# Optimization experiments

Hardware: AMD Instinct MI355X
Metric: run time of the kernel (lower is better)

Reference implementation:

```python
import jax, jax.numpy as jnp
from jax import lax
import numpy as np

EPS = 0.1          # DBSCAN radius (init arg eps)
MIN_SAMPLES = 5    # DBSCAN min_samples (init arg min_samples)
NC_MAX = 512       # fixed padded cluster budget (8 per dim * 64 dims)


def _dbscan_1d(x):
    """Exact 1-D DBSCAN on a vector x of shape (N,).
    Returns (labels, n_clusters). labels[i] in [-1, n_clusters), -1 = noise.
    Clusters are numbered in ascending value order (canonical deterministic
    relabeling of sklearn's discovery order). Border points are attached to
    the nearest core point (ties -> left)."""
    n = x.shape[0]
    order = jnp.argsort(x)
    xs = x[order]
    # core test: #points within [xs-eps, xs+eps] >= min_samples
    hi = jnp.searchsorted(xs, xs + EPS, side='right')
    lo = jnp.searchsorted(xs, xs - EPS, side='left')
    core = (hi - lo) >= MIN_SAMPLES
    inf = jnp.inf
    core_vals = jnp.where(core, xs, -inf)
    run_max = lax.cummax(core_vals, axis=0)                 # nearest core value to the left (incl self)
    prev_core_val = jnp.concatenate([jnp.full((1,), -inf, xs.dtype), run_max[:-1]])
    # a core point starts a new cluster iff no core point within eps on its left
    new_cluster = core & ((xs - prev_core_val) > EPS)
    starts = jnp.cumsum(new_cluster.astype(jnp.int32))
    cid = starts - 1                                        # cluster id carried along sorted order
    ncl = starts[-1]
    # nearest core on the left / right (values and their cluster ids)
    left_cid = lax.cummax(jnp.where(core, cid, -1), axis=0)
    left_val = run_max
    right_cid = lax.cummin(jnp.where(core, cid, n + 1), axis=0, reverse=True)
    right_val = lax.cummin(jnp.where(core, xs, inf), axis=0, reverse=True)
    dl = xs - left_val
    dr = right_val - xs
    border_cid = jnp.where(dl <= dr, left_cid, right_cid)
    border_ok = jnp.minimum(dl, dr) <= EPS
    lab_sorted = jnp.where(core, cid, jnp.where(border_ok, border_cid, -1))
    labels = jnp.zeros_like(lab_sorted).at[order].set(lab_sorted)  # unsort to original node order
    return labels, ncl


def setup_inputs() -> dict:
    key = jax.random.key(0)
    features = jax.random.normal(key, (8, 16384, 64), dtype=jnp.float32)
    return {"features": features}


def reference(features):
    B, N, D = features.shape
    xt = jnp.transpose(features, (0, 2, 1))                  # (B, D, N)
    labels, ncl = jax.vmap(jax.vmap(_dbscan_1d))(xt)         # (B, D, N), (B, D)
    off = jnp.cumsum(ncl, axis=1) - ncl                      # exclusive prefix: global cluster offset per dim
    glb = jnp.where(labels >= 0, labels + off[:, :, None], -1)
    # noise / overflow -> dump into padding column NC_MAX, sliced off below
    lbl = jnp.where(glb >= 0, jnp.minimum(glb, NC_MAX), NC_MAX)
    inc = jnp.zeros((B, N, NC_MAX + 1), features.dtype)
    b_ix = jnp.arange(B)[:, None, None]
    n_ix = jnp.arange(N)[None, None, :]
    inc = inc.at[b_ix, n_ix, lbl].set(1.0)                   # scatter cluster membership
    return inc[:, :, :NC_MAX]                                # (B, N, NC_MAX) padded incidence matrix
```

## Files before the change

### kernel.cpp

```cpp
#include <hip/hip_runtime.h>

#define NPTS   16384
#define NDIM   64
#define NBATCH 8
#define TB     1024
#define VPT    16
#define NB     6144
#define BPT    6
#define NW     (NB/2)
#define EPSF   0.1f
#define MINS   5
#define NCMAX  512
#define BIGI   0x3fffffff

__device__ __forceinline__ int phys(int i) { return i ^ ((i >> 5) & 15); }

__device__ __forceinline__ int binof(float x, float mn, float inv) {
  float fb = (x - mn) * inv;
  int b = (int)fb;
  if (fb < 0.f) b = 0;
  if (b > NB - 1) b = NB - 1;
  return b;
}
__device__ __forceinline__ int pk_get(unsigned w, int odd) {
  return (int)((w >> (odd << 4)) & 0xffffu);
}

__global__ void ktrans(const float* __restrict__ f, float* __restrict__ xt) {
  __shared__ float tile[64][65];
  int blk = blockIdx.x;
  int b   = blk >> 8;
  int n0  = (blk & 255) << 6;
  for (int i = threadIdx.x; i < 64 * 64; i += 256) {
    int n = i >> 6, d = i & 63;
    tile[n][d] = f[((size_t)b * NPTS + n0 + n) * NDIM + d];
  }
  __syncthreads();
  for (int i = threadIdx.x; i < 64 * 64; i += 256) {
    int d = i >> 6, n = i & 63;
    xt[((size_t)b * NDIM + d) * NPTS + n0 + n] = tile[n][d];
  }
}

struct FS { int h; float f; float l; int c; };
__device__ __forceinline__ FS fsid() { FS r; r.h = 0; r.f = 0.f; r.l = 0.f; r.c = 0; return r; }
__device__ __forceinline__ FS fscomb(FS a, FS b) {
  FS r;
  r.h = a.h | b.h;
  r.f = a.h ? a.f : b.f;
  r.l = b.h ? b.l : a.l;
  int gap = (a.h && b.h && ((b.f - a.l) > EPSF)) ? 1 : 0;
  r.c = a.c + b.c + gap;
  return r;
}

__global__ void __launch_bounds__(TB) kdbscan(const float* __restrict__ xt,
                                              short* __restrict__ labels,
                                              int* __restrict__ nclg) {
  const int tid  = threadIdx.x;
  const int lane = tid & 63;
  const int wid  = tid >> 6;
  const int bd   = blockIdx.x;
  const float* __restrict__ x = xt + (size_t)bd * NPTS;

  __shared__ float xs[NPTS];
  __shared__ unsigned offsp[NW];
  __shared__ float wmn[16], wmx[16];
  __shared__ unsigned wsum[16];
  __shared__ int   sh[16];  __shared__ float sf[16], sl[16]; __shared__ int sc[16];
  __shared__ int   wri[16]; __shared__ float wrv[16];
  unsigned* histp = (unsigned*)xs;
  int* labi = (int*)xs;

  float v[VPT];
  float mn = INFINITY, mx = -INFINITY;
  #pragma unroll
  for (int s = 0; s < VPT; ++s) {
    v[s] = x[tid + s * TB];
    mn = fminf(mn, v[s]); mx = fmaxf(mx, v[s]);
  }
  for (int d = 1; d < 64; d <<= 1) {
    mn = fminf(mn, __shfl_xor(mn, d));
    mx = fmaxf(mx, __shfl_xor(mx, d));
  }
  if (lane == 0) { wmn[wid] = mn; wmx[wid] = mx; }
  __syncthreads();
  mn = wmn[0]; mx = wmx[0];
  for (int w = 1; w < 16; ++w) { mn = fminf(mn, wmn[w]); mx = fmaxf(mx, wmx[w]); }
  float range = mx - mn;
  float inv = (range > 0.f) ? ((float)NB / range) : 0.f;

  for (int i = tid; i < NW; i += TB) histp[i] = 0u;
  __syncthreads();
  #pragma unroll
  for (int s = 0; s < VPT; ++s) {
    int b = binof(v[s], mn, inv);
    atomicAdd(&histp[b >> 1], 1u << ((b & 1) << 4));
  }
  __syncthreads();

  {
    unsigned loc[BPT];
    unsigned run = 0;
    const int bbase = tid * BPT;
    #pragma unroll
    for (int j = 0; j < BPT; ++j) {
      int b = bbase + j;
      unsigned c = (histp[b >> 1] >> ((b & 1) << 4)) & 0xffffu;
      loc[j] = run; run += c;
    }
    unsigned incl = run;
    for (int d = 1; d < 64; d <<= 1) {
      unsigned u = __shfl_up(incl, d);
      if (lane >= d) incl += u;
    }
    unsigned exc = __shfl_up(incl, 1);
    if (lane == 0) exc = 0u;
    if (lane == 63) wsum[wid] = incl;
    __syncthreads();
    unsigned wb = 0;
    for (int w = 0; w < wid; ++w) wb += wsum[w];
    unsigned tb0 = wb + exc;
    #pragma unroll
    for (int k = 0; k < BPT / 2; ++k) {
      unsigned a  = tb0 + loc[2 * k];
      unsigned b2 = tb0 + loc[2 * k + 1];
      offsp[(bbase >> 1) + k] = a | (b2 << 16);
    }
  }
  __syncthreads();

  int pos[VPT];
  #pragma unroll
  for (int s = 0; s < VPT; ++s) {
    int b = binof(v[s], mn, inv);
    unsigned old = atomicAdd(&offsp[b >> 1], 1u << ((b & 1) << 4));
    int p = pk_get(old, b & 1);
    pos[s] = p;
    xs[phys(p)] = v[s];
  }
  __syncthreads();

  int tgt[VPT];
  #pragma unroll
  for (int s = 0; s < VPT; ++s) {
    float vv = v[s];
    int pp = pos[s];
    int b  = binof(vv, mn, inv);
    int e0 = pk_get(offsp[b >> 1], b & 1);
    int s0 = b ? pk_get(offsp[(b - 1) >> 1], (b - 1) & 1) : 0;
    int r = 0;
    for (int j = s0; j < e0; ++j) {
      float xj = xs[phys(j)];
      r += (xj < vv || (xj == vv && j < pp)) ? 1 : 0;
    }
    tgt[s] = s0 + r;
  }
  __syncthreads();

  #pragma unroll
  for (int s = 0; s < VPT; ++s) xs[phys(tgt[s])] = v[s];
  __syncthreads();

  const int p0 = tid * VPT;
  float wa[9];
  #pragma unroll
  for (int k = 0; k < 9; ++k) {
    int i = p0 - 4 + k;
    wa[k] = (i < 0) ? -INFINITY : xs[phys(i)];
  }
  unsigned coremask = 0u;
  FS ch = fsid();
  int fi = BIGI; float fv = 0.f;
  #pragma unroll
  for (int s = 0; s < VPT; ++s) {
    float xi = wa[4];
    float lo = xi - EPSF, hi2 = xi + EPSF;
    bool core = false;
    #pragma unroll
    for (int t = 0; t < MINS; ++t)
      core |= (wa[4 - t] >= lo) && (wa[8 - t] <= hi2);
    if (core) {
      coremask |= (1u << s);
      if (!ch.h) { ch.h = 1; ch.f = xi; }
      else if ((xi - ch.l) > EPSF) ++ch.c;
      ch.l = xi;
      if (fi == BIGI) { fi = p0 + s; fv = xi; }
    }
    #pragma unroll
    for (int k = 0; k < 8; ++k) wa[k] = wa[k + 1];
    int nx = p0 + s + 5;
    wa[8] = (nx < NPTS) ? xs[phys(nx)] : INFINITY;
  }

  FS cur = ch;
  for (int d = 1; d < 64; d <<= 1) {
    FS u;
    u.h = __shfl_up(cur.h, d);
    u.f = __shfl_up(cur.f, d);
    u.l = __shfl_up(cur.l, d);
    u.c = __shfl_up(cur.c, d);
    FS cmb = fscomb(u, cur);
    if (lane >= d) cur = cmb;
  }
  FS exs;
  exs.h = __shfl_up(cur.h, 1);
  exs.f = __shfl_up(cur.f, 1);
  exs.l = __shfl_up(cur.l, 1);
  exs.c = __shfl_up(cur.c, 1);
  if (lane == 0) exs = fsid();
  if (lane == 63) { sh[wid] = cur.h; sf[wid] = cur.f; sl[wid] = cur.l; sc[wid] = cur.c; }
  __syncthreads();
  FS pre = fsid();
  for (int w2 = 0; w2 < wid; ++w2) {
    FS t; t.h = sh[w2]; t.f = sf[w2]; t.l = sl[w2]; t.c = sc[w2];
    pre = fscomb(pre, t);
  }
  FS sp = fscomb(pre, exs);

  int ri = fi; float rv = fv;
  for (int d = 1; d < 64; d <<= 1) {
    int ui = __shfl_down(ri, d); float uv = __shfl_down(rv, d);
    if (lane < 64 - d && ui < ri) { ri = ui; rv = uv; }
  }
  int Ri = __shfl_down(ri, 1); float Rv = __shfl_down(rv, 1);
  if (lane == 63) Ri = BIGI;
  if (lane == 0) { wri[wid] = ri; wrv[wid] = rv; }
  __syncthreads();
  for (int w2 = wid + 1; w2 < 16; ++w2)
    if (wri[w2] < Ri) { Ri = wri[w2]; Rv = wrv[w2]; }

  float P  = sp.h ? sp.l : -INFINITY;
  int starts = sp.h ? (sp.c + 1) : 0;
  #pragma unroll
  for (int s = 0; s < VPT; ++s) {
    int i = p0 + s;
    float xi = xs[phys(i)];
    int lb;
    if ((coremask >> s) & 1u) {
      if ((xi - P) > EPSF) ++starts;
      P = xi;
      lb = starts - 1;
    } else {
      float dl = xi - P;
      unsigned hb = coremask >> (s + 1);
      float Rv2; bool has;
      if (hb) { int j = s + 1 + __builtin_ctz(hb); Rv2 = xs[phys(p0 + j)]; has = true; }
      else    { Rv2 = Rv; has = (Ri < NPTS); }
      float dr = has ? (Rv2 - xi) : INFINITY;
      lb = -1;
      if (fminf(dl, dr) <= EPSF)
        lb = (dl <= dr) ? (starts - 1)
                        : (starts - 1 + (((Rv2 - P) > EPSF) ? 1 : 0));
    }
    labi[phys(i)] = lb;
  }
  if (tid == TB - 1) nclg[bd] = starts;
  __syncthreads();

  #pragma unroll
  for (int s = 0; s < VPT; ++s)
    labels[(size_t)bd * NPTS + tid + s * TB] = (short)labi[phys(tgt[s])];
}

__global__ void koffs(const int* __restrict__ ncl, int* __restrict__ colmap) {
  int lane = threadIdx.x & 63;
  int b    = threadIdx.x >> 6;
  int vcnt = ncl[b * 64 + lane];
  int incl = vcnt;
  for (int d = 1; d < 64; d <<= 1) {
    int u = __shfl_up(incl, d);
    if (lane >= d) incl += u;
  }
  int off = incl - vcnt;
  int* cm = colmap + b * NCMAX;
  for (int k = lane; k < NCMAX; k += 64) cm[k] = -1;
  __syncthreads();
  for (int k = 0; k < vcnt; ++k) {
    int col = off + k;
    if (col < NCMAX) cm[col] = lane | (k << 8);
  }
}

__global__ void __launch_bounds__(TB) kout(const short* __restrict__ labels,
                                           const int* __restrict__ colmap,
                                           float* __restrict__ out) {
  const int tid  = threadIdx.x;
  const int lane = tid & 63;
  const int wid  = tid >> 6;
  const int b    = blockIdx.x >> 5;
  const int n0   = (blockIdx.x & 31) * 512 + wid * 32;

  int cm[8];
  const int* cmb = colmap + b * NCMAX;
  #pragma unroll
  for (int k = 0; k < 8; ++k) {
    int col = (k < 4) ? (lane * 4 + k) : (256 + lane * 4 + (k - 4));
    cm[k] = cmb[col];
  }
  const short* lb_b = labels + (size_t)b * NDIM * NPTS;

  for (int r = 0; r < 32; ++r) {
    int n = n0 + r;
    float o[8];
    #pragma unroll
    for (int k = 0; k < 8; ++k) {
      int m = cm[k];
      float val = 0.f;
      if (m >= 0) {
        int d  = m & 255;
        int kk = m >> 8;
        val = (lb_b[(size_t)d * NPTS + n] == (short)kk) ? 1.0f : 0.0f;
      }
      o[k] = val;
    }
    float4* op = (float4*)(out + ((size_t)b * NPTS + n) * NCMAX);
    op[lane]      = make_float4(o[0], o[1], o[2], o[3]);
    op[64 + lane] = make_float4(o[4], o[5], o[6], o[7]);
  }
}

extern "C" void kernel_launch(void* const* d_in, const int* in_sizes, int n_in,
                              void* d_out, int out_size, void* d_ws, size_t ws_size,
                              hipStream_t stream) {
  const float* feat = (const float*)d_in[0];
  float* out = (float*)d_out;

  char* ws = (char*)d_ws;
  size_t xt_b   = (size_t)NBATCH * NPTS * NDIM * 4;
  size_t lbl_b  = (size_t)NBATCH * NPTS * NDIM * 2;
  float* xt     = (float*)ws;
  short* labels = (short*)(ws + xt_b);
  int*   ncl    = (int*)(ws + xt_b + lbl_b);
  int*   colmap = ncl + NBATCH * NDIM;

  ktrans  <<<NBATCH * (NPTS / 64), 256, 0, stream>>>(feat, xt);
  kdbscan <<<NBATCH * NDIM, TB, 0, stream>>>(xt, labels, ncl);
  koffs   <<<1, 512, 0, stream>>>(ncl, colmap);
  kout    <<<NBATCH * 32, TB, 0, stream>>>(labels, colmap, out);
}
```

Before: 184.5 us.

## Fold cluster offset kernel into output kernel and enlarge histogram bins

Removes the separate single-block koffs launch. Each kout block now computes its batch's column map in LDS from the per-dimension cluster counts. The counting sort gets more bins (8192), so each bin holds fewer points and the in-bin rank scan is shorter. Shared memory is repacked so the small scratch arrays alias xs and the histogram array, with an extra barrier added. This adds redundant per-block prefix work in kout and relies on the aliasing being safe.

Result: faster. 179.0 us (-3.0%).

```diff
diff --git a/kernel.cpp b/kernel.cpp
--- a/kernel.cpp
+++ b/kernel.cpp
@@ -5,9 +5,10 @@
 #define NBATCH 8
 #define TB     1024
 #define VPT    16
-#define NB     6144
-#define BPT    6
+#define NB     8192
+#define BPT    8
 #define NW     (NB/2)
+#define WPT    4
 #define EPSF   0.1f
 #define MINS   5
 #define NCMAX  512
@@ -64,13 +65,17 @@
   const float* __restrict__ x = xt + (size_t)bd * NPTS;
 
   __shared__ float xs[NPTS];
-  __shared__ unsigned offsp[NW];
-  __shared__ float wmn[16], wmx[16];
-  __shared__ unsigned wsum[16];
-  __shared__ int   sh[16];  __shared__ float sf[16], sl[16]; __shared__ int sc[16];
-  __shared__ int   wri[16]; __shared__ float wrv[16];
-  unsigned* histp = (unsigned*)xs;
-  int* labi = (int*)xs;
+  __shared__ unsigned A[NW];
+  float*    wmn  = xs;
+  float*    wmx  = xs + 16;
+  unsigned* wsum = (unsigned*)xs + 32;
+  int*      sh   = (int*)A;
+  float*    sf   = (float*)A + 16;
+  float*    sl   = (float*)A + 32;
+  int*      sc   = (int*)A + 48;
+  int*      wri  = (int*)A + 64;
+  float*    wrv  = (float*)A + 80;
+  int*      labi = (int*)xs;
 
   float v[VPT];
   float mn = INFINITY, mx = -INFINITY;
@@ -89,24 +94,27 @@
   for (int w = 1; w < 16; ++w) { mn = fminf(mn, wmn[w]); mx = fmaxf(mx, wmx[w]); }
   float range = mx - mn;
   float inv = (range > 0.f) ? ((float)NB / range) : 0.f;
-
-  for (int i = tid; i < NW; i += TB) histp[i] = 0u;
+  __syncthreads();
+
+  for (int i = tid; i < NW; i += TB) A[i] = 0u;
   __syncthreads();
   #pragma unroll
   for (int s = 0; s < VPT; ++s) {
     int b = binof(v[s], mn, inv);
-    atomicAdd(&histp[b >> 1], 1u << ((b & 1) << 4));
+    atomicAdd(&A[b >> 1], 1u << ((b & 1) << 4));
   }
   __syncthreads();
 
   {
+    const int wbase = tid * WPT;
+    unsigned wv[WPT];
+    #pragma unroll
+    for (int k = 0; k < WPT; ++k) wv[k] = A[wbase + k];
     unsigned loc[BPT];
     unsigned run = 0;
-    const int bbase = tid * BPT;
     #pragma unroll
     for (int j = 0; j < BPT; ++j) {
-      int b = bbase + j;
-      unsigned c = (histp[b >> 1] >> ((b & 1) << 4)) & 0xffffu;
+      unsigned c = (wv[j >> 1] >> ((j & 1) << 4)) & 0xffffu;
       loc[j] = run; run += c;
     }
     unsigned incl = run;
@@ -122,11 +130,8 @@
     for (int w = 0; w < wid; ++w) wb += wsum[w];
     unsigned tb0 = wb + exc;
     #pragma unroll
-    for (int k = 0; k < BPT / 2; ++k) {
-      unsigned a  = tb0 + loc[2 * k];
-      unsigned b2 = tb0 + loc[2 * k + 1];
-      offsp[(bbase >> 1) + k] = a | (b2 << 16);
-    }
+    for (int k = 0; k < WPT; ++k)
+      A[wbase + k] = (tb0 + loc[2 * k]) | ((tb0 + loc[2 * k + 1]) << 16);
   }
   __syncthreads();
 
@@ -134,7 +139,7 @@
   #pragma unroll
   for (int s = 0; s < VPT; ++s) {
     int b = binof(v[s], mn, inv);
-    unsigned old = atomicAdd(&offsp[b >> 1], 1u << ((b & 1) << 4));
+    unsigned old = atomicAdd(&A[b >> 1], 1u << ((b & 1) << 4));
     int p = pk_get(old, b & 1);
     pos[s] = p;
     xs[phys(p)] = v[s];
@@ -144,11 +149,10 @@
   int tgt[VPT];
   #pragma unroll
   for (int s = 0; s < VPT; ++s) {
-    float vv = v[s];
-    int pp = pos[s];
+    float vv = v[s]; int pp = pos[s];
     int b  = binof(vv, mn, inv);
-    int e0 = pk_get(offsp[b >> 1], b & 1);
-    int s0 = b ? pk_get(offsp[(b - 1) >> 1], (b - 1) & 1) : 0;
+    int e0 = pk_get(A[b >> 1], b & 1);
+    int s0 = b ? pk_get(A[(b - 1) >> 1], (b - 1) & 1) : 0;
     int r = 0;
     for (int j = s0; j < e0; ++j) {
       float xj = xs[phys(j)];
@@ -263,27 +267,8 @@
     labels[(size_t)bd * NPTS + tid + s * TB] = (short)labi[phys(tgt[s])];
 }
 
-__global__ void koffs(const int* __restrict__ ncl, int* __restrict__ colmap) {
-  int lane = threadIdx.x & 63;
-  int b    = threadIdx.x >> 6;
-  int vcnt = ncl[b * 64 + lane];
-  int incl = vcnt;
-  for (int d = 1; d < 64; d <<= 1) {
-    int u = __shfl_up(incl, d);
-    if (lane >= d) incl += u;
-  }
-  int off = incl - vcnt;
-  int* cm = colmap + b * NCMAX;
-  for (int k = lane; k < NCMAX; k += 64) cm[k] = -1;
-  __syncthreads();
-  for (int k = 0; k < vcnt; ++k) {
-    int col = off + k;
-    if (col < NCMAX) cm[col] = lane | (k << 8);
-  }
-}
-
 __global__ void __launch_bounds__(TB) kout(const short* __restrict__ labels,
-                                           const int* __restrict__ colmap,
+                                           const int* __restrict__ ncl,
                                            float* __restrict__ out) {
   const int tid  = threadIdx.x;
   const int lane = tid & 63;
@@ -291,12 +276,29 @@
   const int b    = blockIdx.x >> 5;
   const int n0   = (blockIdx.x & 31) * 512 + wid * 32;
 
+  __shared__ int cmLDS[NCMAX];
+  for (int k = tid; k < NCMAX; k += TB) cmLDS[k] = -1;
+  __syncthreads();
+  if (tid < 64) {
+    int vcnt = ncl[b * 64 + tid];
+    int incl = vcnt;
+    for (int d = 1; d < 64; d <<= 1) {
+      int u = __shfl_up(incl, d);
+      if (tid >= d) incl += u;
+    }
+    int off = incl - vcnt;
+    for (int k = 0; k < vcnt; ++k) {
+      int col = off + k;
+      if (col < NCMAX) cmLDS[col] = tid | (k << 8);
+    }
+  }
+  __syncthreads();
+
   int cm[8];
-  const int* cmb = colmap + b * NCMAX;
   #pragma unroll
   for (int k = 0; k < 8; ++k) {
     int col = (k < 4) ? (lane * 4 + k) : (256 + lane * 4 + (k - 4));
-    cm[k] = cmb[col];
+    cm[k] = cmLDS[col];
   }
   const short* lb_b = labels + (size_t)b * NDIM * NPTS;
 
@@ -332,10 +334,8 @@
   float* xt     = (float*)ws;
   short* labels = (short*)(ws + xt_b);
   int*   ncl    = (int*)(ws + xt_b + lbl_b);
-  int*   colmap = ncl + NBATCH * NDIM;
 
   ktrans  <<<NBATCH * (NPTS / 64), 256, 0, stream>>>(feat, xt);
   kdbscan <<<NBATCH * NDIM, TB, 0, stream>>>(xt, labels, ncl);
-  koffs   <<<1, 512, 0, stream>>>(ncl, colmap);
-  kout    <<<NBATCH * 32, TB, 0, stream>>>(labels, colmap, out);
-}
+  kout    <<<NBATCH * 32, TB, 0, stream>>>(labels, ncl, out);
+}
```
